# Kernel optimization log

Measured on AMD Instinct MI355X. Metric: run time of the kernel, lower is better.

Reference implementation:

```python
import jax, jax.numpy as jnp
import numpy as np

N_NODES = 50000
NEG_SLOPE = 0.2


def gat_layer(x, src, dst, w_src, w_dst, att_src, att_dst, bias):
    """Single-head PyG-style GATConv (bipartite weights, same x for src/dst)."""
    xs = x @ w_src                      # [N, C] messages (source projection)
    xd = x @ w_dst                      # [N, C] destination projection
    a_s = xs @ att_src                  # [N] per-node src attention logit
    a_d = xd @ att_dst                  # [N] per-node dst attention logit
    e = jax.nn.leaky_relu(a_s[src] + a_d[dst], NEG_SLOPE)   # [E]
    # segment softmax over edges grouped by destination node
    m = jax.ops.segment_max(e, dst, num_segments=N_NODES)    # [N]
    ex = jnp.exp(e - m[dst])
    denom = jax.ops.segment_sum(ex, dst, num_segments=N_NODES)  # [N]
    alpha = ex / denom[dst]             # [E]
    out = jax.ops.segment_sum(alpha[:, None] * xs[src], dst, num_segments=N_NODES)
    return out + bias


def setup_inputs() -> dict:
    key = jax.random.key(0)
    ks = jax.random.split(key, 12)
    d_in, hid, out = 256, 128, 128
    inv = lambda d: 1.0 / np.sqrt(d)
    x = jax.random.normal(ks[0], (N_NODES, d_in), dtype=jnp.float32)
    edge_index = jax.random.randint(ks[1], (2, 800000), 0, N_NODES, dtype=jnp.int32)
    return {
        "x": x,
        "edge_index": edge_index,
        "w1_src": jax.random.normal(ks[2], (d_in, hid), jnp.float32) * inv(d_in),
        "w1_dst": jax.random.normal(ks[3], (d_in, hid), jnp.float32) * inv(d_in),
        "att1_src": jax.random.normal(ks[4], (hid,), jnp.float32) * inv(hid),
        "att1_dst": jax.random.normal(ks[5], (hid,), jnp.float32) * inv(hid),
        "b1": jnp.zeros((hid,), jnp.float32),
        "w2_src": jax.random.normal(ks[6], (hid, out), jnp.float32) * inv(hid),
        "w2_dst": jax.random.normal(ks[7], (hid, out), jnp.float32) * inv(hid),
        "att2_src": jax.random.normal(ks[8], (out,), jnp.float32) * inv(out),
        "att2_dst": jax.random.normal(ks[9], (out,), jnp.float32) * inv(out),
        "b2": jnp.zeros((out,), jnp.float32),
    }


def reference(x, edge_index, w1_src, w1_dst, att1_src, att1_dst, b1,
              w2_src, w2_dst, att2_src, att2_dst, b2):
    # add self loops once (GATConv default add_self_loops=True)
    loop = jnp.arange(N_NODES, dtype=edge_index.dtype)
    src = jnp.concatenate([edge_index[0], loop])
    dst = jnp.concatenate([edge_index[1], loop])
    h = gat_layer(x, src, dst, w1_src, w1_dst, att1_src, att1_dst, b1)
    h = jax.nn.relu(h)
    return gat_layer(h, src, dst, w2_src, w2_dst, att2_src, att2_dst, b2)
```

## Files before the change

### kernel.cpp

```cpp
#include <hip/hip_runtime.h>

#define NN 50000
#define MAXD 64
#define NEG_SLOPE 0.2f

typedef _Float16 half8 __attribute__((ext_vector_type(8)));
typedef _Float16 half2v __attribute__((ext_vector_type(2)));
typedef float floatx4 __attribute__((ext_vector_type(4)));

__global__ __launch_bounds__(256) void init_kernel(
    const float* __restrict__ w1s, const float* __restrict__ a1s,
    const float* __restrict__ w1d, const float* __restrict__ a1d,
    const float* __restrict__ w2s, const float* __restrict__ a2s,
    const float* __restrict__ w2d, const float* __restrict__ a2d,
    float* u1, float* v1, float* u2, float* v2, int din, int* cnt) {
  int b = blockIdx.x, tid = threadIdx.x;
  if (b < 4) {
    const float *w, *a;
    float* o;
    int d;
    if (b == 0) { w = w1s; a = a1s; o = u1; d = din; }
    else if (b == 1) { w = w1d; a = a1d; o = v1; d = din; }
    else if (b == 2) { w = w2s; a = a2s; o = u2; d = 128; }
    else { w = w2d; a = a2d; o = v2; d = 128; }
    if (tid < d) {
      float s = 0.f;
      for (int j = 0; j < 128; ++j) s += w[tid * 128 + j] * a[j];
      o[tid] = s;
    }
  } else {
    int i = (b - 4) * 256 + tid;
    if (i < NN) cnt[i] = 0;
  }
}


__global__ __launch_bounds__(256) void mega_kernel(
    const int* __restrict__ src, const int* __restrict__ dst,
    int* cnt, int* seg, int e, int G_SCAT,
    const float* __restrict__ w1s,
    const float* __restrict__ u1, const float* __restrict__ v1,
    float* a_s, float* a_d,
    const float* __restrict__ x, _Float16* __restrict__ C, int M, int G_GEMM) {
  constexpr int K = 256, KP = 72;
  __shared__ _Float16 Bt[128 * KP];
  int bid = blockIdx.x, tid = threadIdx.x;
  if (bid < G_SCAT) {
    int i0 = (bid * 256 + tid) * 8;
    int total = e + NN;
#pragma unroll
    for (int j = 0; j < 8; ++j) {
      int i = i0 + j;
      if (i < total) {
        int d, s;
        if (i < e) { d = dst[i]; s = src[i]; }
        else       { d = i - e;  s = d; }
        int r = atomicAdd(&cnt[d], 1);
        if (r < MAXD) seg[(size_t)d * MAXD + r] = s;
      }
    }
  } else if (bid < G_SCAT + G_GEMM) {
    int gb = bid - G_SCAT;
    int lane = tid & 63, wave = tid >> 6;
    int row_base = gb * 64 + wave * 16;
    int lr = lane & 15, lk = lane >> 4;
    floatx4 acc[8];
#pragma unroll
    for (int q = 0; q < 8; ++q) acc[q] = {0.f, 0.f, 0.f, 0.f};
    for (int kc = 0; kc < K; kc += 64) {
      for (int idx = tid; idx < 128 * 64; idx += 256) {
        int k = idx >> 7, c = idx & 127;
        Bt[c * KP + k] = (_Float16)w1s[(size_t)(kc + k) * 128 + c];
      }
      __syncthreads();
#pragma unroll
      for (int k0 = 0; k0 < 64; k0 += 32) {
        int row = row_base + lr;
        half8 a = {0, 0, 0, 0, 0, 0, 0, 0};
        if (row < M) {
          const float* ap = x + (size_t)row * K + kc + k0 + lk * 8;
          float4 f0 = *reinterpret_cast<const float4*>(ap);
          float4 f1 = *reinterpret_cast<const float4*>(ap + 4);
          a = half8{(_Float16)f0.x, (_Float16)f0.y, (_Float16)f0.z, (_Float16)f0.w,
                    (_Float16)f1.x, (_Float16)f1.y, (_Float16)f1.z, (_Float16)f1.w};
        }
        half8 b[8];
#pragma unroll
        for (int q = 0; q < 8; ++q)
          b[q] = *reinterpret_cast<const half8*>(&Bt[(q * 16 + lr) * KP + k0 + lk * 8]);
#pragma unroll
        for (int q = 0; q < 8; ++q)
          acc[q] = __builtin_amdgcn_mfma_f32_16x16x32_f16(a, b[q], acc[q], 0, 0, 0);
      }
      __syncthreads();
    }
#pragma unroll
    for (int q = 0; q < 8; ++q)
#pragma unroll
      for (int r = 0; r < 4; ++r) {
        int row = row_base + lk * 4 + r;
        if (row < M) C[(size_t)row * 128 + q * 16 + lr] = (_Float16)acc[q][r];
      }
  } else {
    int wid = (bid - G_SCAT - G_GEMM) * 4 + (tid >> 6);
    int lane = tid & 63;
    if (wid >= NN) return;
    const float* xr = x + (size_t)wid * 256 + lane * 4;
    float4 xv = *reinterpret_cast<const float4*>(xr);
    float4 uu = *reinterpret_cast<const float4*>(u1 + lane * 4);
    float4 vv = *reinterpret_cast<const float4*>(v1 + lane * 4);
    float s1 = xv.x * uu.x + xv.y * uu.y + xv.z * uu.z + xv.w * uu.w;
    float s2 = xv.x * vv.x + xv.y * vv.y + xv.z * vv.z + xv.w * vv.w;
#pragma unroll
    for (int off = 32; off; off >>= 1) {
      s1 += __shfl_xor(s1, off);
      s2 += __shfl_xor(s2, off);
    }
    if (lane == 0) { a_s[wid] = s1; a_d[wid] = s2; }
  }
}

__global__ __launch_bounds__(256) void agg1_kernel(
    const int* __restrict__ cnt, int* __restrict__ seg,
    const float* __restrict__ a_s, const float* __restrict__ a_d,
    const _Float16* __restrict__ xs, const float* __restrict__ bias,
    _Float16* __restrict__ outp, int n) {
  int wid = (blockIdx.x * blockDim.x + threadIdx.x) >> 6;
  int lane = threadIdx.x & 63;
  if (wid >= n) return;
  int L = cnt[wid];
  L = L < MAXD ? L : MAXD;
  int* srow = seg + (size_t)wid * MAXD;

  int v = (lane < L) ? srow[lane] : 0x7fffffff;
#pragma unroll
  for (int k = 2; k <= 64; k <<= 1) {
#pragma unroll
    for (int j = k >> 1; j > 0; j >>= 1) {
      int other = __shfl_xor(v, j);
      bool dir = ((lane & k) == 0);
      bool lower = ((lane & j) == 0);
      int mn = v < other ? v : other;
      int mx = v < other ? other : v;
      v = (dir == lower) ? mn : mx;
    }
  }
  if (lane < L) srow[lane] = v;

  int g = lane >> 3, lr = lane & 7;
  float ad = a_d[wid];
  float denom = 0.f;
  float acc[16];
#pragma unroll
  for (int j = 0; j < 16; ++j) acc[j] = 0.f;

  auto idx_at = [&](int s_) -> int {
    int val = __shfl(v, s_ & 63);
    return (s_ < L) ? val : -1;
  };

  int slot = g;
  int s_cur = idx_at(slot);
  int slot2 = slot + 8;
  int s_next = idx_at(slot2);
  half8 c0, c1;
  float as_c = 0.f;
  if (s_cur >= 0) {
    const _Float16* pr = &xs[(size_t)s_cur * 128 + lr * 16];
    c0 = *reinterpret_cast<const half8*>(pr);
    c1 = *reinterpret_cast<const half8*>(pr + 8);
    as_c = a_s[s_cur];
  }
  while (s_cur >= 0) {
    half8 n0, n1;
    float as_n = 0.f;
    if (s_next >= 0) {
      const _Float16* pr = &xs[(size_t)s_next * 128 + lr * 16];
      n0 = *reinterpret_cast<const half8*>(pr);
      n1 = *reinterpret_cast<const half8*>(pr + 8);
      as_n = a_s[s_next];
    }
    int slot3 = slot2 + 8;
    int s_nx2 = idx_at(slot3);

    float e = as_c + ad;
    e = e > 0.f ? e : NEG_SLOPE * e;
    float w = __expf(e);
    denom += w;
#pragma unroll
    for (int j = 0; j < 8; ++j) {
      acc[j] += w * (float)c0[j];
      acc[8 + j] += w * (float)c1[j];
    }
    s_cur = s_next; c0 = n0; c1 = n1; as_c = as_n;
    s_next = s_nx2; slot2 = slot3;
  }
  denom += __shfl_xor(denom, 8);
  denom += __shfl_xor(denom, 16);
  denom += __shfl_xor(denom, 32);
#pragma unroll
  for (int j = 0; j < 16; ++j) {
    acc[j] += __shfl_xor(acc[j], 8);
    acc[j] += __shfl_xor(acc[j], 16);
    acc[j] += __shfl_xor(acc[j], 32);
  }
  if (g == 0) {
    float inv = 1.0f / denom;
    half8 h0, h1;
#pragma unroll
    for (int j = 0; j < 8; ++j) {
      float o0 = acc[j] * inv + bias[lr * 16 + j];
      float o1 = acc[8 + j] * inv + bias[lr * 16 + 8 + j];
      h0[j] = (_Float16)fmaxf(o0, 0.f);
      h1[j] = (_Float16)fmaxf(o1, 0.f);
    }
    _Float16* op = &outp[(size_t)wid * 128 + lr * 16];
    *reinterpret_cast<half8*>(op) = h0;
    *reinterpret_cast<half8*>(op + 8) = h1;
  }
}

__global__ __launch_bounds__(256) void fused2_kernel(
    const _Float16* __restrict__ A, const float* __restrict__ B,
    _Float16* __restrict__ C, int M, int G_GEMM,
    const _Float16* __restrict__ xin, const float* __restrict__ u,
    const float* __restrict__ v, float* a_s, float* a_d) {
  constexpr int K = 128, KP = 72;
  __shared__ _Float16 Bt[128 * KP];
  int bid = blockIdx.x, tid = threadIdx.x;
  if (bid < G_GEMM) {
    __builtin_amdgcn_s_setprio(1);
    int lane = tid & 63, wave = tid >> 6;
    int row_base = bid * 64 + wave * 16;
    int lr = lane & 15, lk = lane >> 4;
    floatx4 acc[8];
#pragma unroll
    for (int q = 0; q < 8; ++q) acc[q] = {0.f, 0.f, 0.f, 0.f};
    for (int kc = 0; kc < K; kc += 64) {
      for (int idx = tid; idx < 128 * 64; idx += 256) {
        int k = idx >> 7, c = idx & 127;
        Bt[c * KP + k] = (_Float16)B[(size_t)(kc + k) * 128 + c];
      }
      __syncthreads();
#pragma unroll
      for (int k0 = 0; k0 < 64; k0 += 32) {
        int row = row_base + lr;
        half8 a = {0, 0, 0, 0, 0, 0, 0, 0};
        if (row < M) a = *reinterpret_cast<const half8*>(&A[(size_t)row * K + kc + k0 + lk * 8]);
        half8 b[8];
#pragma unroll
        for (int q = 0; q < 8; ++q)
          b[q] = *reinterpret_cast<const half8*>(&Bt[(q * 16 + lr) * KP + k0 + lk * 8]);
#pragma unroll
        for (int q = 0; q < 8; ++q)
          acc[q] = __builtin_amdgcn_mfma_f32_16x16x32_f16(a, b[q], acc[q], 0, 0, 0);
      }
      __syncthreads();
    }
#pragma unroll
    for (int q = 0; q < 8; ++q)
#pragma unroll
      for (int r = 0; r < 4; ++r) {
        int row = row_base + lk * 4 + r;
        if (row < M) C[(size_t)row * 128 + q * 16 + lr] = (_Float16)acc[q][r];
      }
    __builtin_amdgcn_s_setprio(0);
  } else {
    int wid = (bid - G_GEMM) * 4 + (tid >> 6);
    int lane = tid & 63;
    if (wid >= NN) return;
    float s1, s2;
    const half2v* xr = reinterpret_cast<const half2v*>(&xin[(size_t)wid * 128]);
    {
      int i = lane;
      half2v xv = xr[i];
      float x0 = (float)xv[0], x1 = (float)xv[1];
      s1 = x0 * u[2 * i] + x1 * u[2 * i + 1];
      s2 = x0 * v[2 * i] + x1 * v[2 * i + 1];
    }
#pragma unroll
    for (int off = 32; off; off >>= 1) {
      s1 += __shfl_xor(s1, off);
      s2 += __shfl_xor(s2, off);
    }
    if (lane == 0) { a_s[wid] = s1; a_d[wid] = s2; }
  }
}

__global__ __launch_bounds__(256) void agg2_kernel(
    const int* __restrict__ cnt, const int* __restrict__ seg,
    const float* __restrict__ a_s, const float* __restrict__ a_d,
    const _Float16* __restrict__ xs, const float* __restrict__ bias,
    float* __restrict__ outp, int n) {
  int wid = (blockIdx.x * blockDim.x + threadIdx.x) >> 6;
  int lane = threadIdx.x & 63;
  if (wid >= n) return;
  int g = lane >> 3, lr = lane & 7;
  int L = cnt[wid];
  L = L < MAXD ? L : MAXD;
  const int* srow = seg + (size_t)wid * MAXD;
  float ad = a_d[wid];

  float denom = 0.f;
  float acc[16];
#pragma unroll
  for (int j = 0; j < 16; ++j) acc[j] = 0.f;

  int i = g;
  int s_cur = (i < L) ? srow[i] : -1;
  int i2 = i + 8;
  int s_next = (i2 < L) ? srow[i2] : -1;
  half8 c0, c1;
  float as_c = 0.f;
  if (s_cur >= 0) {
    const _Float16* pr = &xs[(size_t)s_cur * 128 + lr * 16];
    c0 = *reinterpret_cast<const half8*>(pr);
    c1 = *reinterpret_cast<const half8*>(pr + 8);
    as_c = a_s[s_cur];
  }
  while (s_cur >= 0) {
    half8 n0, n1;
    float as_n = 0.f;
    if (s_next >= 0) {
      const _Float16* pr = &xs[(size_t)s_next * 128 + lr * 16];
      n0 = *reinterpret_cast<const half8*>(pr);
      n1 = *reinterpret_cast<const half8*>(pr + 8);
      as_n = a_s[s_next];
    }
    int i3 = i2 + 8;
    int s_nx2 = (i3 < L) ? srow[i3] : -1;

    float e = as_c + ad;
    e = e > 0.f ? e : NEG_SLOPE * e;
    float w = __expf(e);
    denom += w;
#pragma unroll
    for (int j = 0; j < 8; ++j) {
      acc[j] += w * (float)c0[j];
      acc[8 + j] += w * (float)c1[j];
    }
    s_cur = s_next; c0 = n0; c1 = n1; as_c = as_n;
    s_next = s_nx2; i2 = i3;
  }
  denom += __shfl_xor(denom, 8);
  denom += __shfl_xor(denom, 16);
  denom += __shfl_xor(denom, 32);
#pragma unroll
  for (int j = 0; j < 16; ++j) {
    acc[j] += __shfl_xor(acc[j], 8);
    acc[j] += __shfl_xor(acc[j], 16);
    acc[j] += __shfl_xor(acc[j], 32);
  }
  if (g == 0) {
    float inv = 1.0f / denom;
    float o[16];
#pragma unroll
    for (int j = 0; j < 16; ++j) o[j] = acc[j] * inv + bias[lr * 16 + j];
    float* op = &outp[(size_t)wid * 128 + lr * 16];
#pragma unroll
    for (int q = 0; q < 4; ++q) {
      float4 f = make_float4(o[q * 4], o[q * 4 + 1], o[q * 4 + 2], o[q * 4 + 3]);
      *reinterpret_cast<float4*>(op + q * 4) = f;
    }
  }
}

extern "C" void kernel_launch(void* const* d_in, const int* in_sizes, int n_in,
                              void* d_out, int out_size, void* d_ws, size_t ws_size,
                              hipStream_t stream) {
  const float* x        = (const float*)d_in[0];
  const int*   eidx     = (const int*)d_in[1];
  const float* w1_src   = (const float*)d_in[2];
  const float* w1_dst   = (const float*)d_in[3];
  const float* att1_src = (const float*)d_in[4];
  const float* att1_dst = (const float*)d_in[5];
  const float* b1       = (const float*)d_in[6];
  const float* w2_src   = (const float*)d_in[7];
  const float* w2_dst   = (const float*)d_in[8];
  const float* att2_src = (const float*)d_in[9];
  const float* att2_dst = (const float*)d_in[10];
  const float* b2       = (const float*)d_in[11];

  const int E = in_sizes[1] / 2;
  const int DIN = in_sizes[0] / NN;
  const int* src = eidx;
  const int* dst = eidx + E;

  _Float16* h_h = (_Float16*)d_out;
  float*    out = (float*)d_out;

  char* ws = (char*)d_ws;
  size_t off = 0;
  auto alloc = [&](size_t bytes) -> void* {
    void* p = ws + off;
    off = (off + bytes + 255) & ~(size_t)255;
    return p;
  };
  _Float16* xs_h = (_Float16*)alloc((size_t)NN * 128 * sizeof(_Float16));
  float* a_s     = (float*)alloc((size_t)NN * sizeof(float));
  float* a_d     = (float*)alloc((size_t)NN * sizeof(float));
  int*   cnt     = (int*)alloc((size_t)NN * sizeof(int));
  int*   seg     = (int*)alloc((size_t)NN * MAXD * sizeof(int));
  float* u1      = (float*)alloc(256 * sizeof(float));
  float* v1      = (float*)alloc(256 * sizeof(float));
  float* u2      = (float*)alloc(256 * sizeof(float));
  float* v2      = (float*)alloc(256 * sizeof(float));

  const int G_SCAT = ((E + NN) / 8 + 255) / 256;
  const int G_GEMM = (NN + 63) / 64;
  const int G_LOG  = (NN + 3) / 4;
  const int wave_blocks = (NN * 64 + 255) / 256;

  init_kernel<<<4 + (NN + 255) / 256, 256, 0, stream>>>(
      w1_src, att1_src, w1_dst, att1_dst, w2_src, att2_src, w2_dst, att2_dst,
      u1, v1, u2, v2, DIN, cnt);

  mega_kernel<<<G_SCAT + G_GEMM + G_LOG, 256, 0, stream>>>(
      src, dst, cnt, seg, E, G_SCAT,
      w1_src, u1, v1, a_s, a_d, x, xs_h, NN, G_GEMM);

  agg1_kernel<<<wave_blocks, 256, 0, stream>>>(cnt, seg, a_s, a_d, xs_h, b1, h_h, NN);

  fused2_kernel<<<G_GEMM + G_LOG, 256, 0, stream>>>(
      h_h, w2_src, xs_h, NN, G_GEMM, h_h, u2, v2, a_s, a_d);

  agg2_kernel<<<wave_blocks, 256, 0, stream>>>(cnt, seg, a_s, a_d, xs_h, b2, out, NN);
}
```

Baseline: 169.1 us.

## Restructure GAT pipeline: fold attention projections into scatter/agg kernels, move sort to separate pass

Replaces the init kernel with a memset. The u/v attention-vector projections move into the scatter+GEMM mega kernel. Segment sorting and the layer-1 logits move into a new kernel, and the layer-2 logits are computed in agg1's epilogue from the fp32 relu output, so a separate logit pass over h is no longer needed. The aim is to remove redundant passes and shorten the critical path. In exchange there is an extra sort/logit kernel launch, and the layer-2 GEMM loses its co-scheduled logit blocks.

```diff
diff --git a/kernel.cpp b/kernel.cpp
--- a/kernel.cpp
+++ b/kernel.cpp
@@ -8,39 +8,15 @@
 typedef _Float16 half2v __attribute__((ext_vector_type(2)));
 typedef float floatx4 __attribute__((ext_vector_type(4)));
 
-__global__ __launch_bounds__(256) void init_kernel(
+
+__global__ __launch_bounds__(256) void mega_kernel(
+    const int* __restrict__ src, const int* __restrict__ dst,
+    int* cnt, int* seg, int e, int G_SCAT,
     const float* __restrict__ w1s, const float* __restrict__ a1s,
     const float* __restrict__ w1d, const float* __restrict__ a1d,
     const float* __restrict__ w2s, const float* __restrict__ a2s,
     const float* __restrict__ w2d, const float* __restrict__ a2d,
-    float* u1, float* v1, float* u2, float* v2, int din, int* cnt) {
-  int b = blockIdx.x, tid = threadIdx.x;
-  if (b < 4) {
-    const float *w, *a;
-    float* o;
-    int d;
-    if (b == 0) { w = w1s; a = a1s; o = u1; d = din; }
-    else if (b == 1) { w = w1d; a = a1d; o = v1; d = din; }
-    else if (b == 2) { w = w2s; a = a2s; o = u2; d = 128; }
-    else { w = w2d; a = a2d; o = v2; d = 128; }
-    if (tid < d) {
-      float s = 0.f;
-      for (int j = 0; j < 128; ++j) s += w[tid * 128 + j] * a[j];
-      o[tid] = s;
-    }
-  } else {
-    int i = (b - 4) * 256 + tid;
-    if (i < NN) cnt[i] = 0;
-  }
-}
-
-
-__global__ __launch_bounds__(256) void mega_kernel(
-    const int* __restrict__ src, const int* __restrict__ dst,
-    int* cnt, int* seg, int e, int G_SCAT,
-    const float* __restrict__ w1s,
-    const float* __restrict__ u1, const float* __restrict__ v1,
-    float* a_s, float* a_d,
+    float* u1, float* v1, float* u2, float* v2,
     const float* __restrict__ x, _Float16* __restrict__ C, int M, int G_GEMM) {
   constexpr int K = 256, KP = 72;
   __shared__ _Float16 Bt[128 * KP];
@@ -59,8 +35,22 @@
         if (r < MAXD) seg[(size_t)d * MAXD + r] = s;
       }
     }
-  } else if (bid < G_SCAT + G_GEMM) {
-    int gb = bid - G_SCAT;
+  } else if (bid < G_SCAT + 4) {
+    int b = bid - G_SCAT;
+    const float *w, *a;
+    float* o;
+    int d;
+    if (b == 0) { w = w1s; a = a1s; o = u1; d = K; }
+    else if (b == 1) { w = w1d; a = a1d; o = v1; d = K; }
+    else if (b == 2) { w = w2s; a = a2s; o = u2; d = 128; }
+    else { w = w2d; a = a2d; o = v2; d = 128; }
+    if (tid < d) {
+      float s = 0.f;
+      for (int j = 0; j < 128; ++j) s += w[tid * 128 + j] * a[j];
+      o[tid] = s;
+    }
+  } else {
+    int gb = bid - G_SCAT - 4;
     int lane = tid & 63, wave = tid >> 6;
     int row_base = gb * 64 + wave * 16;
     int lr = lane & 15, lk = lane >> 4;
@@ -101,14 +91,46 @@
         int row = row_base + lk * 4 + r;
         if (row < M) C[(size_t)row * 128 + q * 16 + lr] = (_Float16)acc[q][r];
       }
+  }
+}
+
+__global__ __launch_bounds__(256) void ls_kernel(
+    const int* __restrict__ cnt, int* seg, int G_SORT,
+    const float* __restrict__ x, const float* __restrict__ u,
+    const float* __restrict__ v, float* a_s, float* a_d) {
+  int bid = blockIdx.x, tid = threadIdx.x;
+  if (bid < G_SORT) {
+    int wid = bid * 4 + (tid >> 6);
+    int lane = tid & 63;
+    if (wid < NN) {
+      int L = cnt[wid];
+      L = L < MAXD ? L : MAXD;
+      if (L > 1) {
+        int* srow = seg + (size_t)wid * MAXD;
+        int v2_ = (lane < L) ? srow[lane] : 0x7fffffff;
+#pragma unroll
+        for (int k = 2; k <= 64; k <<= 1) {
+#pragma unroll
+          for (int j = k >> 1; j > 0; j >>= 1) {
+            int other = __shfl_xor(v2_, j);
+            bool dir = ((lane & k) == 0);
+            bool lower = ((lane & j) == 0);
+            int mn = v2_ < other ? v2_ : other;
+            int mx = v2_ < other ? other : v2_;
+            v2_ = (dir == lower) ? mn : mx;
+          }
+        }
+        if (lane < L) srow[lane] = v2_;
+      }
+    }
   } else {
-    int wid = (bid - G_SCAT - G_GEMM) * 4 + (tid >> 6);
+    int wid = (bid - G_SORT) * 4 + (tid >> 6);
     int lane = tid & 63;
     if (wid >= NN) return;
     const float* xr = x + (size_t)wid * 256 + lane * 4;
     float4 xv = *reinterpret_cast<const float4*>(xr);
-    float4 uu = *reinterpret_cast<const float4*>(u1 + lane * 4);
-    float4 vv = *reinterpret_cast<const float4*>(v1 + lane * 4);
+    float4 uu = *reinterpret_cast<const float4*>(u + lane * 4);
+    float4 vv = *reinterpret_cast<const float4*>(v + lane * 4);
     float s1 = xv.x * uu.x + xv.y * uu.y + xv.z * uu.z + xv.w * uu.w;
     float s2 = xv.x * vv.x + xv.y * vv.y + xv.z * vv.z + xv.w * vv.w;
 #pragma unroll
@@ -121,48 +143,30 @@
 }
 
 __global__ __launch_bounds__(256) void agg1_kernel(
-    const int* __restrict__ cnt, int* __restrict__ seg,
+    const int* __restrict__ cnt, const int* __restrict__ seg,
     const float* __restrict__ a_s, const float* __restrict__ a_d,
     const _Float16* __restrict__ xs, const float* __restrict__ bias,
+    const float* __restrict__ u2, const float* __restrict__ v2,
+    float* __restrict__ a_s2, float* __restrict__ a_d2,
     _Float16* __restrict__ outp, int n) {
   int wid = (blockIdx.x * blockDim.x + threadIdx.x) >> 6;
   int lane = threadIdx.x & 63;
   if (wid >= n) return;
+  int g = lane >> 3, lr = lane & 7;
   int L = cnt[wid];
   L = L < MAXD ? L : MAXD;
-  int* srow = seg + (size_t)wid * MAXD;
-
-  int v = (lane < L) ? srow[lane] : 0x7fffffff;
-#pragma unroll
-  for (int k = 2; k <= 64; k <<= 1) {
-#pragma unroll
-    for (int j = k >> 1; j > 0; j >>= 1) {
-      int other = __shfl_xor(v, j);
-      bool dir = ((lane & k) == 0);
-      bool lower = ((lane & j) == 0);
-      int mn = v < other ? v : other;
-      int mx = v < other ? other : v;
-      v = (dir == lower) ? mn : mx;
-    }
-  }
-  if (lane < L) srow[lane] = v;
-
-  int g = lane >> 3, lr = lane & 7;
+  const int* srow = seg + (size_t)wid * MAXD;
   float ad = a_d[wid];
+
   float denom = 0.f;
   float acc[16];
 #pragma unroll
   for (int j = 0; j < 16; ++j) acc[j] = 0.f;
 
-  auto idx_at = [&](int s_) -> int {
-    int val = __shfl(v, s_ & 63);
-    return (s_ < L) ? val : -1;
-  };
-
-  int slot = g;
-  int s_cur = idx_at(slot);
-  int slot2 = slot + 8;
-  int s_next = idx_at(slot2);
+  int i = g;
+  int s_cur = (i < L) ? srow[i] : -1;
+  int i2 = i + 8;
+  int s_next = (i2 < L) ? srow[i2] : -1;
   half8 c0, c1;
   float as_c = 0.f;
   if (s_cur >= 0) {
@@ -180,8 +184,8 @@
       n1 = *reinterpret_cast<const half8*>(pr + 8);
       as_n = a_s[s_next];
     }
-    int slot3 = slot2 + 8;
-    int s_nx2 = idx_at(slot3);
+    int i3 = i2 + 8;
+    int s_nx2 = (i3 < L) ? srow[i3] : -1;
 
     float e = as_c + ad;
     e = e > 0.f ? e : NEG_SLOPE * e;
@@ -193,7 +197,7 @@
       acc[8 + j] += w * (float)c1[j];
     }
     s_cur = s_next; c0 = n0; c1 = n1; as_c = as_n;
-    s_next = s_nx2; slot2 = slot3;
+    s_next = s_nx2; i2 = i3;
   }
   denom += __shfl_xor(denom, 8);
   denom += __shfl_xor(denom, 16);
@@ -206,85 +210,74 @@
   }
   if (g == 0) {
     float inv = 1.0f / denom;
+    float ho[16];
     half8 h0, h1;
 #pragma unroll
+    for (int j = 0; j < 16; ++j) {
+      float o = acc[j] * inv + bias[lr * 16 + j];
+      ho[j] = fmaxf(o, 0.f);
+    }
+#pragma unroll
     for (int j = 0; j < 8; ++j) {
-      float o0 = acc[j] * inv + bias[lr * 16 + j];
-      float o1 = acc[8 + j] * inv + bias[lr * 16 + 8 + j];
-      h0[j] = (_Float16)fmaxf(o0, 0.f);
-      h1[j] = (_Float16)fmaxf(o1, 0.f);
+      h0[j] = (_Float16)ho[j];
+      h1[j] = (_Float16)ho[8 + j];
     }
     _Float16* op = &outp[(size_t)wid * 128 + lr * 16];
     *reinterpret_cast<half8*>(op) = h0;
     *reinterpret_cast<half8*>(op + 8) = h1;
-  }
-}
-
-__global__ __launch_bounds__(256) void fused2_kernel(
+    float p1 = 0.f, p2 = 0.f;
+#pragma unroll
+    for (int j = 0; j < 16; ++j) {
+      p1 += ho[j] * u2[lr * 16 + j];
+      p2 += ho[j] * v2[lr * 16 + j];
+    }
+    p1 += __shfl_xor(p1, 1); p2 += __shfl_xor(p2, 1);
+    p1 += __shfl_xor(p1, 2); p2 += __shfl_xor(p2, 2);
+    p1 += __shfl_xor(p1, 4); p2 += __shfl_xor(p2, 4);
+    if (lr == 0) { a_s2[wid] = p1; a_d2[wid] = p2; }
+  }
+}
+
+__global__ __launch_bounds__(256) void gemm2_kernel(
     const _Float16* __restrict__ A, const float* __restrict__ B,
-    _Float16* __restrict__ C, int M, int G_GEMM,
-    const _Float16* __restrict__ xin, const float* __restrict__ u,
-    const float* __restrict__ v, float* a_s, float* a_d) {
+    _Float16* __restrict__ C, int M) {
   constexpr int K = 128, KP = 72;
   __shared__ _Float16 Bt[128 * KP];
   int bid = blockIdx.x, tid = threadIdx.x;
-  if (bid < G_GEMM) {
-    __builtin_amdgcn_s_setprio(1);
-    int lane = tid & 63, wave = tid >> 6;
-    int row_base = bid * 64 + wave * 16;
-    int lr = lane & 15, lk = lane >> 4;
-    floatx4 acc[8];
-#pragma unroll
-    for (int q = 0; q < 8; ++q) acc[q] = {0.f, 0.f, 0.f, 0.f};
-    for (int kc = 0; kc < K; kc += 64) {
-      for (int idx = tid; idx < 128 * 64; idx += 256) {
-        int k = idx >> 7, c = idx & 127;
-        Bt[c * KP + k] = (_Float16)B[(size_t)(kc + k) * 128 + c];
-      }
-      __syncthreads();
-#pragma unroll
-      for (int k0 = 0; k0 < 64; k0 += 32) {
-        int row = row_base + lr;
-        half8 a = {0, 0, 0, 0, 0, 0, 0, 0};
-        if (row < M) a = *reinterpret_cast<const half8*>(&A[(size_t)row * K + kc + k0 + lk * 8]);
-        half8 b[8];
-#pragma unroll
-        for (int q = 0; q < 8; ++q)
-          b[q] = *reinterpret_cast<const half8*>(&Bt[(q * 16 + lr) * KP + k0 + lk * 8]);
-#pragma unroll
-        for (int q = 0; q < 8; ++q)
-          acc[q] = __builtin_amdgcn_mfma_f32_16x16x32_f16(a, b[q], acc[q], 0, 0, 0);
-      }
-      __syncthreads();
-    }
-#pragma unroll
-    for (int q = 0; q < 8; ++q)
-#pragma unroll
-      for (int r = 0; r < 4; ++r) {
-        int row = row_base + lk * 4 + r;
-        if (row < M) C[(size_t)row * 128 + q * 16 + lr] = (_Float16)acc[q][r];
-      }
-    __builtin_amdgcn_s_setprio(0);
-  } else {
-    int wid = (bid - G_GEMM) * 4 + (tid >> 6);
-    int lane = tid & 63;
-    if (wid >= NN) return;
-    float s1, s2;
-    const half2v* xr = reinterpret_cast<const half2v*>(&xin[(size_t)wid * 128]);
-    {
-      int i = lane;
-      half2v xv = xr[i];
-      float x0 = (float)xv[0], x1 = (float)xv[1];
-      s1 = x0 * u[2 * i] + x1 * u[2 * i + 1];
-      s2 = x0 * v[2 * i] + x1 * v[2 * i + 1];
-    }
-#pragma unroll
-    for (int off = 32; off; off >>= 1) {
-      s1 += __shfl_xor(s1, off);
-      s2 += __shfl_xor(s2, off);
-    }
-    if (lane == 0) { a_s[wid] = s1; a_d[wid] = s2; }
-  }
+  int lane = tid & 63, wave = tid >> 6;
+  int row_base = bid * 64 + wave * 16;
+  int lr = lane & 15, lk = lane >> 4;
+  floatx4 acc[8];
+#pragma unroll
+  for (int q = 0; q < 8; ++q) acc[q] = {0.f, 0.f, 0.f, 0.f};
+  for (int kc = 0; kc < K; kc += 64) {
+    for (int idx = tid; idx < 128 * 64; idx += 256) {
+      int k = idx >> 7, c = idx & 127;
+      Bt[c * KP + k] = (_Float16)B[(size_t)(kc + k) * 128 + c];
+    }
+    __syncthreads();
+#pragma unroll
+    for (int k0 = 0; k0 < 64; k0 += 32) {
+      int row = row_base + lr;
+      half8 a = {0, 0, 0, 0, 0, 0, 0, 0};
+      if (row < M) a = *reinterpret_cast<const half8*>(&A[(size_t)row * K + kc + k0 + lk * 8]);
+      half8 b[8];
+#pragma unroll
+      for (int q = 0; q < 8; ++q)
+        b[q] = *reinterpret_cast<const half8*>(&Bt[(q * 16 + lr) * KP + k0 + lk * 8]);
+#pragma unroll
+      for (int q = 0; q < 8; ++q)
+        acc[q] = __builtin_amdgcn_mfma_f32_16x16x32_f16(a, b[q], acc[q], 0, 0, 0);
+    }
+    __syncthreads();
+  }
+#pragma unroll
+  for (int q = 0; q < 8; ++q)
+#pragma unroll
+    for (int r = 0; r < 4; ++r) {
+      int row = row_base + lk * 4 + r;
+      if (row < M) C[(size_t)row * 128 + q * 16 + lr] = (_Float16)acc[q][r];
+    }
 }
 
 __global__ __launch_bounds__(256) void agg2_kernel(
@@ -382,7 +375,6 @@
   const float* b2       = (const float*)d_in[11];
 
   const int E = in_sizes[1] / 2;
-  const int DIN = in_sizes[0] / NN;
   const int* src = eidx;
   const int* dst = eidx + E;
 
@@ -399,6 +391,8 @@
   _Float16* xs_h = (_Float16*)alloc((size_t)NN * 128 * sizeof(_Float16));
   float* a_s     = (float*)alloc((size_t)NN * sizeof(float));
   float* a_d     = (float*)alloc((size_t)NN * sizeof(float));
+  float* a_s2    = (float*)alloc((size_t)NN * sizeof(float));
+  float* a_d2    = (float*)alloc((size_t)NN * sizeof(float));
   int*   cnt     = (int*)alloc((size_t)NN * sizeof(int));
   int*   seg     = (int*)alloc((size_t)NN * MAXD * sizeof(int));
   float* u1      = (float*)alloc(256 * sizeof(float));
@@ -408,21 +402,23 @@
 
   const int G_SCAT = ((E + NN) / 8 + 255) / 256;
   const int G_GEMM = (NN + 63) / 64;
+  const int G_SORT = (NN + 3) / 4;
   const int G_LOG  = (NN + 3) / 4;
   const int wave_blocks = (NN * 64 + 255) / 256;
 
-  init_kernel<<<4 + (NN + 255) / 256, 256, 0, stream>>>(
+  hipMemsetAsync(cnt, 0, NN * sizeof(int), stream);
+
+  mega_kernel<<<G_SCAT + 4 + G_GEMM, 256, 0, stream>>>(
+      src, dst, cnt, seg, E, G_SCAT,
       w1_src, att1_src, w1_dst, att1_dst, w2_src, att2_src, w2_dst, att2_dst,
-      u1, v1, u2, v2, DIN, cnt);
-
-  mega_kernel<<<G_SCAT + G_GEMM + G_LOG, 256, 0, stream>>>(
-      src, dst, cnt, seg, E, G_SCAT,
-      w1_src, u1, v1, a_s, a_d, x, xs_h, NN, G_GEMM);
-
-  agg1_kernel<<<wave_blocks, 256, 0, stream>>>(cnt, seg, a_s, a_d, xs_h, b1, h_h, NN);
-
-  fused2_kernel<<<G_GEMM + G_LOG, 256, 0, stream>>>(
-      h_h, w2_src, xs_h, NN, G_GEMM, h_h, u2, v2, a_s, a_d);
-
-  agg2_kernel<<<wave_blocks, 256, 0, stream>>>(cnt, seg, a_s, a_d, xs_h, b2, out, NN);
-}
+      u1, v1, u2, v2, x, xs_h, NN, G_GEMM);
+
+  ls_kernel<<<G_SORT + G_LOG, 256, 0, stream>>>(cnt, seg, G_SORT, x, u1, v1, a_s, a_d);
+
+  agg1_kernel<<<wave_blocks, 256, 0, stream>>>(
+      cnt, seg, a_s, a_d, xs_h, b1, u2, v2, a_s2, a_d2, h_h, NN);
+
+  gemm2_kernel<<<G_GEMM, 256, 0, stream>>>(h_h, w2_src, xs_h, NN);
+
+  agg2_kernel<<<wave_blocks, 256, 0, stream>>>(cnt, seg, a_s2, a_d2, xs_h, b2, out, NN);
+}
```

New measurement: 181.3 us. 7.2% more time.
